# Performance work log

Hardware: AMD Instinct MI355X
Metric: run time of the kernel (lower is better)

The kernel has to match this reference:

```python
import jax, jax.numpy as jnp
import numpy as np

LN_EPS = 1e-5
SLOPE = 0.01  # LeakyReLU default

def _ln(x, g, b):
    m = x.mean(-1, keepdims=True)
    v = ((x - m) ** 2).mean(-1, keepdims=True)
    return (x - m) / jnp.sqrt(v + LN_EPS) * g + b

def _leaky(x):
    return jnp.where(x >= 0, x, SLOPE * x)

def _lstm(x_seq, h0, c0, Wih, Whh, bih, bhh):
    # x_seq: [B,S,E]; PyTorch gate order i,f,g,o. Returns (hT, per-step hiddens [B,S,H]).
    gx = jnp.einsum('bse,ge->bsg', x_seq, Wih) + bih + bhh  # precompute input projections
    def step(carry, gxt):
        h, c = carry
        gates = gxt + h @ Whh.T
        i, f, g, o = jnp.split(gates, 4, axis=-1)
        c = jax.nn.sigmoid(f) * c + jax.nn.sigmoid(i) * jnp.tanh(g)
        h = jax.nn.sigmoid(o) * jnp.tanh(c)
        return (h, c), h
    (hT, _), hs = jax.lax.scan(step, (h0, c0), gx.transpose(1, 0, 2))
    return hT, hs.transpose(1, 0, 2)

def setup_inputs() -> dict:
    B, S, NF, E, H, L, C = 256, 1024, 32, 64, 128, 64, 31
    key = jax.random.key(0)
    ks = iter(jax.random.split(key, 40))
    rn = lambda shape, s=0.08: (jax.random.normal(next(ks), shape, jnp.float32) * s)
    d = {}
    d['x'] = jax.random.normal(next(ks), (B, S, NF), jnp.float32)
    d['eps'] = jax.random.normal(next(ks), (B, L), jnp.float32)
    d['init_W'] = rn((E, NF)); d['init_b'] = rn((E,)); d['init_g'] = jnp.ones((E,)); d['init_beta'] = jnp.zeros((E,))
    d['enc_Wih'] = rn((4 * H, E)); d['enc_Whh'] = rn((4 * H, H)); d['enc_bih'] = rn((4 * H,)); d['enc_bhh'] = rn((4 * H,))
    d['mu_W'] = rn((L, H)); d['mu_b'] = rn((L,)); d['mu_g'] = jnp.ones((L,)); d['mu_beta'] = jnp.zeros((L,))
    d['lv_W'] = rn((L, H)); d['lv_b'] = rn((L,)); d['lv_g'] = jnp.ones((L,)); d['lv_beta'] = jnp.zeros((L,))
    d['dec_Wih'] = rn((4 * H, E)); d['dec_Whh'] = rn((4 * H, H)); d['dec_bih'] = rn((4 * H,)); d['dec_bhh'] = rn((4 * H,))
    d['lh_W'] = rn((H, L)); d['lh_b'] = rn((H,)); d['lh_g'] = jnp.ones((H,)); d['lh_beta'] = jnp.zeros((H,))
    d['lc_W'] = rn((H, L)); d['lc_b'] = rn((H,)); d['lc_g'] = jnp.ones((H,)); d['lc_beta'] = jnp.zeros((H,))
    d['act_W'] = rn((C, H)); d['act_b'] = rn((C,))
    d['time_W'] = rn((1, H)); d['time_b'] = rn((1,))
    return d

def reference(x, eps, init_W, init_b, init_g, init_beta,
              enc_Wih, enc_Whh, enc_bih, enc_bhh,
              mu_W, mu_b, mu_g, mu_beta, lv_W, lv_b, lv_g, lv_beta,
              dec_Wih, dec_Whh, dec_bih, dec_bhh,
              lh_W, lh_b, lh_g, lh_beta, lc_W, lc_b, lc_g, lc_beta,
              act_W, act_b, time_W, time_b):
    B = x.shape[0]
    H = enc_Whh.shape[1]
    # init_layers: Linear -> LeakyReLU -> LayerNorm
    x_emb = _ln(_leaky(x @ init_W.T + init_b), init_g, init_beta)  # [B,S,E]
    # encoder LSTM with h0=ones, c0=zeros (as in encode())
    hT, _ = _lstm(x_emb, jnp.ones((B, H), x.dtype), jnp.zeros((B, H), x.dtype),
                  enc_Wih, enc_Whh, enc_bih, enc_bhh)
    mu = _ln(_leaky(hT @ mu_W.T + mu_b), mu_g, mu_beta)
    logvar = _ln(_leaky(hT @ lv_W.T + lv_b), lv_g, lv_beta)
    latent = mu + eps * jnp.exp(0.5 * logvar)
    # decoder init state from latent
    dh0 = _ln(_leaky(latent @ lh_W.T + lh_b), lh_g, lh_beta)
    dc0 = _ln(_leaky(latent @ lc_W.T + lc_b), lc_g, lc_beta)
    # _decode prefix loop (prefix_len=1..S-1, collecting hn) == one scan over x_emb[:, :S-1]
    _, hs = _lstm(x_emb[:, :-1], dh0, dc0, dec_Wih, dec_Whh, dec_bih, dec_bhh)  # [B,S-1,H]
    acts = hs @ act_W.T + act_b   # [B,S-1,C]
    ts = hs @ time_W.T + time_b   # [B,S-1,1]
    return acts, ts, mu, logvar
```

## Files before the change

kernel.cpp:

```cpp
#include <hip/hip_runtime.h>
#include <hip/hip_bf16.h>
#include <type_traits>


#define B_ 256
#define S_ 1024
#define NF_ 32
#define E_ 64
#define H_ 128
#define L_ 64
#define C_ 31

#define ACTS_OFF 0
#define TS_OFF   8118528
#define MU_OFF   8380416
#define LV_OFF   8396800

#define LOG2E  1.44269504f
#define LOG2E2 2.88539008f

typedef __attribute__((ext_vector_type(8))) short short8;
typedef __attribute__((ext_vector_type(4))) float float4v;

__device__ inline unsigned short f2bf(float x){
  union { float f; unsigned u; } a; a.f = x;
  unsigned r = a.u + 0x7FFFu + ((a.u >> 16) & 1u);
  return (unsigned short)(r >> 16);
}
__device__ inline float frcp(float x){
#if __has_builtin(__builtin_amdgcn_rcpf)
  return __builtin_amdgcn_rcpf(x);
#else
  return 1.0f / x;
#endif
}
__device__ inline float fexp2(float x){
#if __has_builtin(__builtin_amdgcn_exp2f)
  return __builtin_amdgcn_exp2f(x);
#else
  return exp2f(x);
#endif
}
__device__ inline float fsig(float x){ return frcp(1.0f + fexp2(-LOG2E*x)); }
__device__ inline float leaky(float x){ return x >= 0.0f ? x : 0.01f*x; }
__device__ inline float wredsum(float v){
  v += __shfl_xor(v, 32, 64);
  v += __shfl_xor(v, 16, 64);
  v += __shfl_xor(v,  8, 64);
  v += __shfl_xor(v,  4, 64);
  v += __shfl_xor(v,  2, 64);
  v += __shfl_xor(v,  1, 64);
  return v;
}

#define INIT_ROWS 16
__global__ __launch_bounds__(256) void init_kernel(
    const float* __restrict__ x, const float* __restrict__ W,
    const float* __restrict__ bias, const float* __restrict__ gam,
    const float* __restrict__ beta, unsigned short* __restrict__ xemb)
{
  if (blockIdx.x == 0 && threadIdx.x < 64)
    xemb[(size_t)S_*B_*E_ + threadIdx.x] = 0;

  const int wave = threadIdx.x >> 6, lane = threadIdx.x & 63;
  float wf[NF_];
  {
    const float4* wr = (const float4*)(W + lane * NF_);
    #pragma unroll
    for (int j = 0; j < NF_/4; ++j){
      float4 t = wr[j];
      wf[4*j+0] = t.x; wf[4*j+1] = t.y; wf[4*j+2] = t.z; wf[4*j+3] = t.w;
    }
  }
  const float bb = bias[lane], gg = gam[lane], be = beta[lane];

  const int r0 = (blockIdx.x * 4 + wave) * INIT_ROWS;
  for (int rr = 0; rr < INIT_ROWS; ++rr){
    const int ru = __builtin_amdgcn_readfirstlane(r0 + rr);
    const int b = ru >> 10, s = ru & 1023;
    const float* xr = x + (size_t)ru * NF_;
    float acc = bb;
    #pragma unroll
    for (int k = 0; k < NF_; ++k)
      acc = fmaf(xr[k], wf[k], acc);
    acc = leaky(acc);
    float m = wredsum(acc) * (1.0f/64.0f);
    float d = acc - m;
    float v = wredsum(d*d) * (1.0f/64.0f);
    float y = d * rsqrtf(v + 1e-5f) * gg + be;
    xemb[((size_t)s * B_ + b) * E_ + lane] = f2bf(y);
  }
}

__global__ __launch_bounds__(512, 2) void mega_kernel(
    const unsigned short* __restrict__ xemb,
    const float* __restrict__ encWih, const float* __restrict__ encWhh,
    const float* __restrict__ encbih, const float* __restrict__ encbhh,
    const float* __restrict__ decWih, const float* __restrict__ decWhh,
    const float* __restrict__ decbih, const float* __restrict__ decbhh,
    const float* __restrict__ eps,
    const float* __restrict__ mu_W, const float* __restrict__ mu_b,
    const float* __restrict__ mu_g, const float* __restrict__ mu_be,
    const float* __restrict__ lv_W, const float* __restrict__ lv_b,
    const float* __restrict__ lv_g, const float* __restrict__ lv_be,
    const float* __restrict__ lh_W, const float* __restrict__ lh_b,
    const float* __restrict__ lh_g, const float* __restrict__ lh_be,
    const float* __restrict__ lc_W, const float* __restrict__ lc_b,
    const float* __restrict__ lc_g, const float* __restrict__ lc_be,
    const float* __restrict__ actW, const float* __restrict__ actB,
    const float* __restrict__ timeW, const float* __restrict__ timeB,
    float* __restrict__ out)
{
  __shared__ unsigned short hbuf[2][16*136];
  __shared__ unsigned short hist[2][16*136];
  __shared__ float shT[4][H_];
  __shared__ float sml[4][2*L_];
  __shared__ float slat[4][L_];
  __shared__ float sdh[4][H_], sdc[4][H_];
  __shared__ float partA[8];

  const int tid = threadIdx.x;
  const int wave = tid >> 6, lane = tid & 63;
  const int q = lane >> 4, c16 = lane & 15;
  const int bt0 = blockIdx.x * 4;
  const int hu = wave * 16 + c16;
  unsigned short* hflat = &hbuf[0][0];
  unsigned short* histf = &hist[0][0];
  const float4v z4 = (float4v){0.0f, 0.0f, 0.0f, 0.0f};
  float zero_f = 0.0f;

  for (int idx = tid; idx < 2*16*136; idx += 512) hflat[idx] = 0;
  __syncthreads();

  const int xb = c16 >> 2, xdt = c16 & 3;
  const unsigned short* xbase = xemb + ((size_t)(bt0 + xb))*E_ + q*8;
  const size_t xrow = (size_t)B_*E_;

  using I0 = std::integral_constant<int,0>;
  using I1 = std::integral_constant<int,1>;
  using I2 = std::integral_constant<int,2>;
  using I3 = std::integral_constant<int,3>;
  auto nop = []{};

  auto run = [&](const float* Wih, const float* Whh, const float* bih,
                 const float* bhh, int T, auto decc){
    constexpr bool DEC = decltype(decc)::value;

    short8 Bf[4][6];
    float bias[4];
    #pragma unroll
    for (int g = 0; g < 4; ++g){
      const int gcol = g*128 + hu;
      bias[g] = bih[gcol] + bhh[gcol];
      #pragma unroll
      for (int kb = 0; kb < 6; ++kb){
        union { short8 v; unsigned short u[8]; } tmp;
        #pragma unroll
        for (int j = 0; j < 8; ++j){
          int k = kb*32 + q*8 + j;
          float wv = (kb < 4) ? Whh[gcol*H_ + k] : Wih[gcol*E_ + (k - H_)];
          tmp.u[j] = f2bf(wv);
        }
        Bf[g][kb] = tmp.v;
      }
    }

    const bool do_head = DEC && (wave < 2);
    short8 Of0 = 0, Of1 = 0, Of2 = 0, Of3 = 0;
    float obias = 0.0f;
    if (do_head){
      const int n = wave*16 + c16;
      obias = (n < C_) ? actB[n] : timeB[0];
      union { short8 v; unsigned short u[8]; } tmp[4];
      #pragma unroll
      for (int kb = 0; kb < 4; ++kb)
        #pragma unroll
        for (int j = 0; j < 8; ++j){
          int k = kb*32 + q*8 + j;
          tmp[kb].u[j] = f2bf((n < C_) ? actW[n*H_ + k] : timeW[k]);
        }
      Of0 = tmp[0].v; Of1 = tmp[1].v; Of2 = tmp[2].v; Of3 = tmp[3].v;
    }
    short8 Ph0 = 0, Ph1 = 0, Ph2 = 0, Ph3 = 0;
    float4v oacc = z4;

    {
      int b = tid >> 7, k = tid & 127;
      hbuf[0][(4*b)*136 + k] = DEC ? f2bf(sdh[b][k]) : (unsigned short)0x3F80;
    }
    float cst = DEC ? sdc[q][hu] : 0.0f;
    __syncthreads();

    auto xwin = [&](int wt)->const unsigned short*{
      int tt = wt + xdt; if (tt > T-1) tt = T-1;
      return xbase + (size_t)tt * xrow;
    };

    float4v gxA[4], gxB[4];
    short8 nx0, nx1;
    { const unsigned short* p = xwin(0);
      nx0 = *(const short8*)p; nx1 = *(const short8*)(p + 32); }
    #pragma unroll
    for (int g = 0; g < 4; ++g){
      float4v t = (float4v){bias[g], bias[g], bias[g], bias[g]};
      t = __builtin_amdgcn_mfma_f32_16x16x32_bf16(nx0, Bf[g][4], t, 0, 0, 0);
      gxA[g] = __builtin_amdgcn_mfma_f32_16x16x32_bf16(nx1, Bf[g][5], t, 0, 0, 0);
    }
    { const unsigned short* p = xwin(4);
      nx0 = *(const short8*)p; nx1 = *(const short8*)(p + 32); }

    short8 Af0 = 0, Af1 = 0, Af2 = 0, Af3 = 0;

    const unsigned short* haR0 = hflat + (c16 & ~3)*136 + q*8;
    const unsigned short* haR1 = haR0 + 2176;
    unsigned short* hw0 = hflat + (4*q)*136 + hu;
    unsigned short* hw1 = hw0 + 2176;

    auto step = [&](int t, auto dtc, float4v (&gxP)[4], auto&& pre, auto&& post){
      constexpr int dt = decltype(dtc)::value;
      const unsigned short* ha = (t & 1) ? haR1 : haR0;
      if ((c16 & 3) == dt){
        Af0 = *(const short8*)(ha);
        Af1 = *(const short8*)(ha + 32);
        Af2 = *(const short8*)(ha + 64);
        Af3 = *(const short8*)(ha + 96);
      }
      pre();

      float4v aA[4], aB[4];
      #pragma unroll
      for (int g = 0; g < 4; ++g)
        aA[g] = __builtin_amdgcn_mfma_f32_16x16x32_bf16(Af0, Bf[g][0], gxP[g], 0, 0, 0);
      #pragma unroll
      for (int g = 0; g < 4; ++g)
        aB[g] = __builtin_amdgcn_mfma_f32_16x16x32_bf16(Af2, Bf[g][2], z4, 0, 0, 0);
      #pragma unroll
      for (int g = 0; g < 4; ++g)
        aA[g] = __builtin_amdgcn_mfma_f32_16x16x32_bf16(Af1, Bf[g][1], aA[g], 0, 0, 0);
      #pragma unroll
      for (int g = 0; g < 4; ++g)
        aB[g] = __builtin_amdgcn_mfma_f32_16x16x32_bf16(Af3, Bf[g][3], aB[g], 0, 0, 0);

      post();

      float gi = aA[0][dt] + aB[0][dt];
      float gf = aA[1][dt] + aB[1][dt];
      float gg = aA[2][dt] + aB[2][dt];
      float go = aA[3][dt] + aB[3][dt];
      float ei  = fexp2(gi * LOG2E);
      float e2g = fexp2(gg * LOG2E2);
      float t1  = (ei * (e2g - 1.0f)) * frcp((1.0f + ei) * (1.0f + e2g));
      float sf  = fsig(gf);
      float c   = fmaf(sf, cst, t1);
      cst = c;
      float eo  = fexp2(go * LOG2E);
      float e2c = fexp2(fminf(c * LOG2E2, 126.0f));
      float h   = (eo * (e2c - 1.0f)) * frcp((1.0f + eo) * (1.0f + e2c));
      unsigned vv;
      asm("v_cvt_pk_bf16_f32 %0, %1, %2" : "=v"(vv) : "v"(h), "v"(zero_f));
      unsigned short hb16 = (unsigned short)vv;
      unsigned short* hw = (t & 1) ? hw0 : hw1;
      hw[0] = hb16;
      if (DEC)
        histf[((t >> 2) & 1)*2176 + (4*q + dt)*136 + hu] = hb16;
      if (!DEC && t == T-1) shT[q][hu] = h;
      __builtin_amdgcn_sched_barrier(0);
      asm volatile("s_waitcnt lgkmcnt(0)" ::: "memory");
      __builtin_amdgcn_s_barrier();
      __builtin_amdgcn_sched_barrier(0);
    };

    auto head_mfma = [&](int par){
      const unsigned short* hb = histf + par*2176 + c16*136 + q*8;
      Ph0 = *(const short8*)(hb);
      Ph1 = *(const short8*)(hb + 32);
      Ph2 = *(const short8*)(hb + 64);
      Ph3 = *(const short8*)(hb + 96);
      float4v o = (float4v){obias, obias, obias, obias};
      o = __builtin_amdgcn_mfma_f32_16x16x32_bf16(Ph0, Of0, o, 0, 0, 0);
      o = __builtin_amdgcn_mfma_f32_16x16x32_bf16(Ph1, Of1, o, 0, 0, 0);
      o = __builtin_amdgcn_mfma_f32_16x16x32_bf16(Ph2, Of2, o, 0, 0, 0);
      o = __builtin_amdgcn_mfma_f32_16x16x32_bf16(Ph3, Of3, o, 0, 0, 0);
      oacc = o;
    };
    auto head_store = [&](int tb, int cnt){
      const int n = wave*16 + c16;
      const size_t bq = (size_t)(bt0 + q);
      if (n < C_){
        #pragma unroll
        for (int r = 0; r < 4; ++r)
          if (r < cnt) out[ACTS_OFF + (bq*(size_t)(S_-1) + (size_t)(tb + r))*C_ + n] = oacc[r];
      } else {
        #pragma unroll
        for (int r = 0; r < 4; ++r)
          if (r < cnt) out[TS_OFF + bq*(size_t)(S_-1) + (size_t)(tb + r)] = oacc[r];
      }
    };

    const int nwin = T >> 2, ntail = T & 3;
    for (int w = 0; w < nwin; ++w){
      const int t0 = w << 2;
      step(t0+0, I0{}, gxA, [&]{
        #pragma unroll
        for (int g = 0; g < 4; ++g){
          float4v tt = (float4v){bias[g], bias[g], bias[g], bias[g]};
          tt = __builtin_amdgcn_mfma_f32_16x16x32_bf16(nx0, Bf[g][4], tt, 0, 0, 0);
          gxB[g] = __builtin_amdgcn_mfma_f32_16x16x32_bf16(nx1, Bf[g][5], tt, 0, 0, 0);
        }
      }, nop);
      step(t0+1, I1{}, gxA, [&]{
        const unsigned short* p = xwin(t0 + 8);
        nx0 = *(const short8*)p; nx1 = *(const short8*)(p + 32);
      }, nop);
      step(t0+2, I2{}, gxA, [&]{
        if (do_head && w > 0) head_mfma((w-1) & 1);
      }, nop);
      step(t0+3, I3{}, gxA, [&]{
        if (do_head && w > 0) head_store((w-1)*4, 4);
      }, [&]{
        #pragma unroll
        for (int g = 0; g < 4; ++g) gxA[g] = gxB[g];
      });
    }
    if (ntail > 0) step(nwin*4+0, I0{}, gxA, [&]{
        if (do_head) head_mfma((nwin-1) & 1);
      }, nop);
    if (ntail > 1) step(nwin*4+1, I1{}, gxA, [&]{
        if (do_head) head_store((nwin-1)*4, 4);
      }, nop);
    if (ntail > 2) step(nwin*4+2, I2{}, gxA, nop, nop);
    if (do_head && ntail > 0){
      head_mfma(nwin & 1);
      head_store(nwin*4, ntail);
    }
  };

  run(encWih, encWhh, encbih, encbhh, S_, std::integral_constant<bool,false>{});

  {
    const int bb = tid >> 7, slot = tid & 127;
    const int unit = slot & 63;
    const bool isLv = slot >= 64;
    const float* W = isLv ? lv_W : mu_W;
    float a = (isLv ? lv_b : mu_b)[unit];
    const float4* wr = (const float4*)(W + unit*H_);
    #pragma unroll 4
    for (int j = 0; j < H_/4; ++j){
      float4 w4 = wr[j];
      a += w4.x*shT[bb][4*j] + w4.y*shT[bb][4*j+1]
         + w4.z*shT[bb][4*j+2] + w4.w*shT[bb][4*j+3];
    }
    a = leaky(a);
    float m = wredsum(a) * (1.0f/L_);
    float d = a - m;
    float v = wredsum(d*d) * (1.0f/L_);
    float y = d * rsqrtf(v + 1e-5f) * (isLv ? lv_g : mu_g)[unit]
            + (isLv ? lv_be : mu_be)[unit];
    out[(isLv ? LV_OFF : MU_OFF) + (size_t)(bt0 + bb)*L_ + unit] = y;
    sml[bb][slot] = y;
    __syncthreads();
    if (!isLv)
      slat[bb][unit] = sml[bb][unit]
                     + eps[(size_t)(bt0 + bb)*L_ + unit] * expf(0.5f*sml[bb][64 + unit]);
    __syncthreads();
    #pragma unroll 1
    for (int which = 0; which < 2; ++which){
      const float* W2 = which ? lc_W : lh_W;
      float p = (which ? lc_b : lh_b)[slot];
      const float4* w2 = (const float4*)(W2 + slot*L_);
      #pragma unroll 4
      for (int j = 0; j < L_/4; ++j){
        float4 w4 = w2[j];
        p += w4.x*slat[bb][4*j] + w4.y*slat[bb][4*j+1]
           + w4.z*slat[bb][4*j+2] + w4.w*slat[bb][4*j+3];
      }
      p = leaky(p);
      float s = wredsum(p);
      if (lane == 0) partA[wave] = s;
      __syncthreads();
      float mean = (partA[2*bb] + partA[2*bb+1]) * (1.0f/H_);
      __syncthreads();
      float dd = p - mean;
      float s2 = wredsum(dd*dd);
      if (lane == 0) partA[wave] = s2;
      __syncthreads();
      float var = (partA[2*bb] + partA[2*bb+1]) * (1.0f/H_);
      __syncthreads();
      float yy = dd * rsqrtf(var + 1e-5f) * (which ? lc_g : lh_g)[slot]
               + (which ? lc_be : lh_be)[slot];
      (which ? sdc : sdh)[bb][slot] = yy;
    }
  }
  __syncthreads();

  run(decWih, decWhh, decbih, decbhh, S_-1, std::integral_constant<bool,true>{});
}

extern "C" void kernel_launch(void* const* d_in, const int* in_sizes, int n_in,
                              void* d_out, int out_size, void* d_ws, size_t ws_size,
                              hipStream_t stream)
{
  (void)in_sizes; (void)n_in; (void)out_size; (void)ws_size;
  const float* x       = (const float*)d_in[0];
  const float* eps     = (const float*)d_in[1];
  const float* init_W  = (const float*)d_in[2];
  const float* init_b  = (const float*)d_in[3];
  const float* init_g  = (const float*)d_in[4];
  const float* init_be = (const float*)d_in[5];
  const float* enc_Wih = (const float*)d_in[6];
  const float* enc_Whh = (const float*)d_in[7];
  const float* enc_bih = (const float*)d_in[8];
  const float* enc_bhh = (const float*)d_in[9];
  const float* mu_W  = (const float*)d_in[10];
  const float* mu_b  = (const float*)d_in[11];
  const float* mu_g  = (const float*)d_in[12];
  const float* mu_be = (const float*)d_in[13];
  const float* lv_W  = (const float*)d_in[14];
  const float* lv_b  = (const float*)d_in[15];
  const float* lv_g  = (const float*)d_in[16];
  const float* lv_be = (const float*)d_in[17];
  const float* dec_Wih = (const float*)d_in[18];
  const float* dec_Whh = (const float*)d_in[19];
  const float* dec_bih = (const float*)d_in[20];
  const float* dec_bhh = (const float*)d_in[21];
  const float* lh_W  = (const float*)d_in[22];
  const float* lh_b  = (const float*)d_in[23];
  const float* lh_g  = (const float*)d_in[24];
  const float* lh_be = (const float*)d_in[25];
  const float* lc_W  = (const float*)d_in[26];
  const float* lc_b  = (const float*)d_in[27];
  const float* lc_g  = (const float*)d_in[28];
  const float* lc_be = (const float*)d_in[29];
  const float* act_W  = (const float*)d_in[30];
  const float* act_b  = (const float*)d_in[31];
  const float* time_W = (const float*)d_in[32];
  const float* time_b = (const float*)d_in[33];
  float* out = (float*)d_out;

  unsigned short* xemb = (unsigned short*)d_ws;

  init_kernel<<<dim3((B_*S_)/(4*INIT_ROWS)), dim3(256), 0, stream>>>(
      x, init_W, init_b, init_g, init_be, xemb);

  mega_kernel<<<dim3(64), dim3(512), 0, stream>>>(
      xemb,
      enc_Wih, enc_Whh, enc_bih, enc_bhh,
      dec_Wih, dec_Whh, dec_bih, dec_bhh,
      eps,
      mu_W, mu_b, mu_g, mu_be,
      lv_W, lv_b, lv_g, lv_be,
      lh_W, lh_b, lh_g, lh_be,
      lc_W, lc_b, lc_g, lc_be,
      act_W, act_b, time_W, time_b,
      out);
}
```

Measured before the change: 1.203 ms.

## Move output head projection out of recurrent loop into separate MFMA kernel

The act/time output projection no longer runs inside the decoder's serial LSTM loop on waves 0-1. Each decoder step now writes its bf16 hidden state to a global workspace buffer, and a new out_kernel computes the projections afterwards with MFMA across all timesteps in parallel. This takes the head loads, MFMAs and scattered stores off the latency-bound recurrence critical path, and it frees the LDS history buffer. In exchange it adds a global store per step, a workspace round trip of roughly 67 MB, and an extra kernel launch.

```diff
diff --git a/kernel.cpp b/kernel.cpp
--- a/kernel.cpp
+++ b/kernel.cpp
@@ -107,12 +107,10 @@
     const float* __restrict__ lh_g, const float* __restrict__ lh_be,
     const float* __restrict__ lc_W, const float* __restrict__ lc_b,
     const float* __restrict__ lc_g, const float* __restrict__ lc_be,
-    const float* __restrict__ actW, const float* __restrict__ actB,
-    const float* __restrict__ timeW, const float* __restrict__ timeB,
+    unsigned short* __restrict__ hs,
     float* __restrict__ out)
 {
   __shared__ unsigned short hbuf[2][16*136];
-  __shared__ unsigned short hist[2][16*136];
   __shared__ float shT[4][H_];
   __shared__ float sml[4][2*L_];
   __shared__ float slat[4][L_];
@@ -125,7 +123,6 @@
   const int bt0 = blockIdx.x * 4;
   const int hu = wave * 16 + c16;
   unsigned short* hflat = &hbuf[0][0];
-  unsigned short* histf = &hist[0][0];
   const float4v z4 = (float4v){0.0f, 0.0f, 0.0f, 0.0f};
   float zero_f = 0.0f;
 
@@ -165,25 +162,6 @@
       }
     }
 
-    const bool do_head = DEC && (wave < 2);
-    short8 Of0 = 0, Of1 = 0, Of2 = 0, Of3 = 0;
-    float obias = 0.0f;
-    if (do_head){
-      const int n = wave*16 + c16;
-      obias = (n < C_) ? actB[n] : timeB[0];
-      union { short8 v; unsigned short u[8]; } tmp[4];
-      #pragma unroll
-      for (int kb = 0; kb < 4; ++kb)
-        #pragma unroll
-        for (int j = 0; j < 8; ++j){
-          int k = kb*32 + q*8 + j;
-          tmp[kb].u[j] = f2bf((n < C_) ? actW[n*H_ + k] : timeW[k]);
-        }
-      Of0 = tmp[0].v; Of1 = tmp[1].v; Of2 = tmp[2].v; Of3 = tmp[3].v;
-    }
-    short8 Ph0 = 0, Ph1 = 0, Ph2 = 0, Ph3 = 0;
-    float4v oacc = z4;
-
     {
       int b = tid >> 7, k = tid & 127;
       hbuf[0][(4*b)*136 + k] = DEC ? f2bf(sdh[b][k]) : (unsigned short)0x3F80;
@@ -215,6 +193,7 @@
     const unsigned short* haR1 = haR0 + 2176;
     unsigned short* hw0 = hflat + (4*q)*136 + hu;
     unsigned short* hw1 = hw0 + 2176;
+    unsigned short* hsp = hs + ((size_t)(bt0 + q))*H_ + hu;
 
     auto step = [&](int t, auto dtc, float4v (&gxP)[4], auto&& pre, auto&& post){
       constexpr int dt = decltype(dtc)::value;
@@ -261,40 +240,12 @@
       unsigned short hb16 = (unsigned short)vv;
       unsigned short* hw = (t & 1) ? hw0 : hw1;
       hw[0] = hb16;
-      if (DEC)
-        histf[((t >> 2) & 1)*2176 + (4*q + dt)*136 + hu] = hb16;
+      if (DEC){ *hsp = hb16; hsp += (size_t)B_*H_; }
       if (!DEC && t == T-1) shT[q][hu] = h;
       __builtin_amdgcn_sched_barrier(0);
       asm volatile("s_waitcnt lgkmcnt(0)" ::: "memory");
       __builtin_amdgcn_s_barrier();
       __builtin_amdgcn_sched_barrier(0);
-    };
-
-    auto head_mfma = [&](int par){
-      const unsigned short* hb = histf + par*2176 + c16*136 + q*8;
-      Ph0 = *(const short8*)(hb);
-      Ph1 = *(const short8*)(hb + 32);
-      Ph2 = *(const short8*)(hb + 64);
-      Ph3 = *(const short8*)(hb + 96);
-      float4v o = (float4v){obias, obias, obias, obias};
-      o = __builtin_amdgcn_mfma_f32_16x16x32_bf16(Ph0, Of0, o, 0, 0, 0);
-      o = __builtin_amdgcn_mfma_f32_16x16x32_bf16(Ph1, Of1, o, 0, 0, 0);
-      o = __builtin_amdgcn_mfma_f32_16x16x32_bf16(Ph2, Of2, o, 0, 0, 0);
-      o = __builtin_amdgcn_mfma_f32_16x16x32_bf16(Ph3, Of3, o, 0, 0, 0);
-      oacc = o;
-    };
-    auto head_store = [&](int tb, int cnt){
-      const int n = wave*16 + c16;
-      const size_t bq = (size_t)(bt0 + q);
-      if (n < C_){
-        #pragma unroll
-        for (int r = 0; r < 4; ++r)
-          if (r < cnt) out[ACTS_OFF + (bq*(size_t)(S_-1) + (size_t)(tb + r))*C_ + n] = oacc[r];
-      } else {
-        #pragma unroll
-        for (int r = 0; r < 4; ++r)
-          if (r < cnt) out[TS_OFF + bq*(size_t)(S_-1) + (size_t)(tb + r)] = oacc[r];
-      }
     };
 
     const int nwin = T >> 2, ntail = T & 3;
@@ -312,27 +263,15 @@
         const unsigned short* p = xwin(t0 + 8);
         nx0 = *(const short8*)p; nx1 = *(const short8*)(p + 32);
       }, nop);
-      step(t0+2, I2{}, gxA, [&]{
-        if (do_head && w > 0) head_mfma((w-1) & 1);
-      }, nop);
-      step(t0+3, I3{}, gxA, [&]{
-        if (do_head && w > 0) head_store((w-1)*4, 4);
-      }, [&]{
+      step(t0+2, I2{}, gxA, nop, nop);
+      step(t0+3, I3{}, gxA, nop, [&]{
         #pragma unroll
         for (int g = 0; g < 4; ++g) gxA[g] = gxB[g];
       });
     }
-    if (ntail > 0) step(nwin*4+0, I0{}, gxA, [&]{
-        if (do_head) head_mfma((nwin-1) & 1);
-      }, nop);
-    if (ntail > 1) step(nwin*4+1, I1{}, gxA, [&]{
-        if (do_head) head_store((nwin-1)*4, 4);
-      }, nop);
+    if (ntail > 0) step(nwin*4+0, I0{}, gxA, nop, nop);
+    if (ntail > 1) step(nwin*4+1, I1{}, gxA, nop, nop);
     if (ntail > 2) step(nwin*4+2, I2{}, gxA, nop, nop);
-    if (do_head && ntail > 0){
-      head_mfma(nwin & 1);
-      head_store(nwin*4, ntail);
-    }
   };
 
   run(encWih, encWhh, encbih, encbhh, S_, std::integral_constant<bool,false>{});
@@ -394,6 +333,55 @@
   __syncthreads();
 
   run(decWih, decWhh, decbih, decbhh, S_-1, std::integral_constant<bool,true>{});
+}
+
+__global__ __launch_bounds__(256) void out_kernel(
+    const unsigned short* __restrict__ hs,
+    const float* __restrict__ actW, const float* __restrict__ actB,
+    const float* __restrict__ timeW, const float* __restrict__ timeB,
+    float* __restrict__ out)
+{
+  const int wave = threadIdx.x >> 6, lane = threadIdx.x & 63;
+  const int quad = lane >> 4, c16 = lane & 15;
+  const int mt = blockIdx.x * 4 + wave;
+  short8 Wf[2][4]; float biasn[2];
+  #pragma unroll
+  for (int ti = 0; ti < 2; ++ti){
+    const int n = ti*16 + c16;
+    biasn[ti] = (n < C_) ? actB[n] : timeB[0];
+    #pragma unroll
+    for (int kb = 0; kb < 4; ++kb){
+      union { short8 v; unsigned short u[8]; } tmp;
+      #pragma unroll
+      for (int j = 0; j < 8; ++j){
+        int k = kb*32 + quad*8 + j;
+        tmp.u[j] = f2bf((n < C_) ? actW[n*H_ + k] : timeW[k]);
+      }
+      Wf[ti][kb] = tmp.v;
+    }
+  }
+  const unsigned short* hp = hs + ((size_t)mt*16 + c16)*H_ + quad*8;
+  float4v acc[2];
+  #pragma unroll
+  for (int ti = 0; ti < 2; ++ti) acc[ti] = (float4v){biasn[ti], biasn[ti], biasn[ti], biasn[ti]};
+  #pragma unroll
+  for (int kb = 0; kb < 4; ++kb){
+    short8 a = *(const short8*)(hp + kb*32);
+    acc[0] = __builtin_amdgcn_mfma_f32_16x16x32_bf16(a, Wf[0][kb], acc[0], 0, 0, 0);
+    acc[1] = __builtin_amdgcn_mfma_f32_16x16x32_bf16(a, Wf[1][kb], acc[1], 0, 0, 0);
+  }
+  #pragma unroll
+  for (int ti = 0; ti < 2; ++ti){
+    const int n = ti*16 + c16;
+    #pragma unroll
+    for (int r = 0; r < 4; ++r){
+      int rr = mt*16 + quad*4 + r;
+      int tt = rr >> 8, b = rr & 255;
+      float v = acc[ti][r];
+      if (n < C_) out[ACTS_OFF + ((size_t)b*1023 + tt)*C_ + n] = v;
+      else        out[TS_OFF + (size_t)b*1023 + tt] = v;
+    }
+  }
 }
 
 extern "C" void kernel_launch(void* const* d_in, const int* in_sizes, int n_in,
@@ -438,6 +426,7 @@
   float* out = (float*)d_out;
 
   unsigned short* xemb = (unsigned short*)d_ws;
+  unsigned short* hs   = xemb + (size_t)S_*B_*E_ + 64;
 
   init_kernel<<<dim3((B_*S_)/(4*INIT_ROWS)), dim3(256), 0, stream>>>(
       x, init_W, init_b, init_g, init_be, xemb);
@@ -451,6 +440,8 @@
       lv_W, lv_b, lv_g, lv_be,
       lh_W, lh_b, lh_g, lh_be,
       lc_W, lc_b, lc_g, lc_be,
-      act_W, act_b, time_W, time_b,
-      out);
-}
+      hs, out);
+
+  out_kernel<<<dim3((B_*(S_-1))/16/4), dim3(256), 0, stream>>>(
+      hs, act_W, act_b, time_W, time_b, out);
+}
```

Result: faster. 1.165 ms (-3.2%).
